# Kernel tuning notes

Measured on AMD Instinct MI355X. Metric: run time of the kernel, lower is better.

## Reference

```python
import jax, jax.numpy as jnp
import numpy as np


def mish(x):
    return x * jnp.tanh(jax.nn.softplus(x))


def setup_inputs() -> dict:
    key = jax.random.key(0)
    k1, k2, k3, k4, k5 = jax.random.split(key, 5)
    B, C, H, W = 16, 256, 128, 128
    sq = max(int(C * 4 * 0.25), 1)  # 256
    return {
        "t": jax.random.normal(k1, (B, C, H, W), dtype=jnp.float32),
        "w_reduce": jax.random.normal(k2, (sq, 4 * C), dtype=jnp.float32) * 0.02,
        "b_reduce": jax.random.normal(k3, (sq,), dtype=jnp.float32) * 0.02,
        "w_expand": jax.random.normal(k4, (4 * C, sq), dtype=jnp.float32) * 0.02,
        "b_expand": jax.random.normal(k5, (4 * C,), dtype=jnp.float32) * 0.02,
    }


def reference(t, w_reduce, b_reduce, w_expand, b_expand):
    B, C, H, W = t.shape
    h, w = H // 2, W // 2
    # Quadrants (views of t)
    x00 = t[:, :, :h, :w]
    x01 = t[:, :, :h, w:]
    x10 = t[:, :, h:, :w]
    x11 = t[:, :, h:, w:]
    # Squeeze: per-quadrant global average pool -> [B, 4C]
    means = jnp.concatenate(
        [q.mean(axis=(2, 3)) for q in (x00, x01, x10, x11)], axis=1
    )
    # 1x1 convs at 1x1 spatial == small GEMMs
    z = mish(means @ w_reduce.T + b_reduce)          # [B, sq]
    gate = jax.nn.sigmoid(z @ w_expand.T + b_expand)  # [B, 4C]
    g = gate.reshape(B, 4, C)[:, :, :, None, None]    # [B,4,C,1,1]
    # out2 = t * gate broadcast back into each quadrant (out=ones in source)
    top = jnp.concatenate([x00 * g[:, 0], x01 * g[:, 1]], axis=3)
    bot = jnp.concatenate([x10 * g[:, 2], x11 * g[:, 3]], axis=3)
    return jnp.concatenate([top, bot], axis=2)
```

## Files before the change

### kernel.cpp

```cpp
#include <hip/hip_runtime.h>
#include <math.h>

namespace {
constexpr int Bx = 16;
constexpr int Cx = 256;
constexpr int Hx = 128;
constexpr int Wx = 128;
constexpr int PLANE = Hx * Wx;
constexpr int NPLANES = Bx * Cx;
constexpr int SQ = 256;
constexpr int C4 = 4 * Cx;
}

__global__ __launch_bounds__(256) void k_qmeans(const float* __restrict__ t,
                                                float* __restrict__ means) {
    const int plane = blockIdx.x;
    const int tid = threadIdx.x;
    const float4* tp = (const float4*)(t + (size_t)plane * PLANE);

    float sTop = 0.f, sBot = 0.f;
#pragma unroll
    for (int i = 0; i < 8; ++i) {
        float4 d = tp[tid + 256 * i];
        sTop += (d.x + d.y) + (d.z + d.w);
    }
#pragma unroll
    for (int i = 8; i < 16; ++i) {
        float4 d = tp[tid + 256 * i];
        sBot += (d.x + d.y) + (d.z + d.w);
    }

#pragma unroll
    for (int m = 1; m <= 8; m <<= 1) {
        sTop += __shfl_xor(sTop, m);
        sBot += __shfl_xor(sBot, m);
    }
    sTop += __shfl_xor(sTop, 32);
    sBot += __shfl_xor(sBot, 32);

    __shared__ float red[4][4];
    const int lane = tid & 63;
    const int wave = tid >> 6;
    const int qc = (tid >> 4) & 1;
    if (lane == 0 || lane == 16) {
        red[qc][wave] = sTop;
        red[2 + qc][wave] = sBot;
    }
    __syncthreads();
    if (tid < 4) {
        const float s = red[tid][0] + red[tid][1] + red[tid][2] + red[tid][3];
        const int b = plane >> 8;
        const int c = plane & 255;
        means[b * C4 + tid * Cx + c] = s * (1.f / (64.f * 64.f));
    }
}

__global__ __launch_bounds__(256) void k_mlp(const float* __restrict__ means,
                                             const float* __restrict__ w_reduce,
                                             const float* __restrict__ b_reduce,
                                             const float* __restrict__ w_expand,
                                             const float* __restrict__ b_expand,
                                             float* __restrict__ gate) {
    const int b = blockIdx.x;
    const int tid = threadIdx.x;
    __shared__ __align__(16) float ms[C4];
    __shared__ __align__(16) float zs[SQ];

#pragma unroll
    for (int i = 0; i < 4; ++i)
        ms[tid + 256 * i] = means[b * C4 + tid + 256 * i];
    __syncthreads();

    {
        float acc = b_reduce[tid];
        const float4* wr = (const float4*)(w_reduce + (size_t)tid * C4);
        const float4* m4 = (const float4*)ms;
#pragma unroll 8
        for (int k = 0; k < C4 / 4; ++k) {
            const float4 w = wr[k];
            const float4 m = m4[k];
            acc += m.x * w.x + m.y * w.y + m.z * w.z + m.w * w.w;
        }
        const float sp = (acc > 20.f) ? acc : log1pf(expf(acc));
        zs[tid] = acc * tanhf(sp);
    }
    __syncthreads();

#pragma unroll
    for (int i = 0; i < 4; ++i) {
        const int j = tid + 256 * i;
        float acc = b_expand[j];
        const float4* we = (const float4*)(w_expand + (size_t)j * SQ);
        const float4* z4 = (const float4*)zs;
#pragma unroll 8
        for (int k = 0; k < SQ / 4; ++k) {
            const float4 w = we[k];
            const float4 z = z4[k];
            acc += z.x * w.x + z.y * w.y + z.z * w.z + z.w * w.w;
        }
        gate[b * C4 + j] = 1.f / (1.f + expf(-acc));
    }
}

__global__ __launch_bounds__(256) void k_apply(const float* __restrict__ t,
                                               const float* __restrict__ gate,
                                               float* __restrict__ out) {
    const int plane = blockIdx.x;
    const int tid = threadIdx.x;
    const int b = plane >> 8;
    const int c = plane & 255;

    const float g0 = gate[b * C4 + 0 * Cx + c];
    const float g1 = gate[b * C4 + 1 * Cx + c];
    const float g2 = gate[b * C4 + 2 * Cx + c];
    const float g3 = gate[b * C4 + 3 * Cx + c];
    const int qc = (tid >> 4) & 1;
    const float gTop = qc ? g1 : g0;
    const float gBot = qc ? g3 : g2;

    const float4* tp = (const float4*)(t + (size_t)plane * PLANE);
    float4* op = (float4*)((float*)out + (size_t)plane * PLANE);
#pragma unroll
    for (int i = 0; i < 16; ++i) {
        float4 d = tp[tid + 256 * i];
        const float g = (i < 8) ? gTop : gBot;
        d.x *= g; d.y *= g; d.z *= g; d.w *= g;
        op[tid + 256 * i] = d;
    }
}

extern "C" void kernel_launch(void* const* d_in, const int* in_sizes, int n_in,
                              void* d_out, int out_size, void* d_ws, size_t ws_size,
                              hipStream_t stream) {
    const float* t        = (const float*)d_in[0];
    const float* w_reduce = (const float*)d_in[1];
    const float* b_reduce = (const float*)d_in[2];
    const float* w_expand = (const float*)d_in[3];
    const float* b_expand = (const float*)d_in[4];
    float* out = (float*)d_out;

    float* means = (float*)d_ws;
    float* gate  = means + Bx * C4;

    k_qmeans<<<NPLANES, 256, 0, stream>>>(t, means);
    k_mlp<<<Bx, 256, 0, stream>>>(means, w_reduce, b_reduce, w_expand, b_expand, gate);
    k_apply<<<NPLANES, 256, 0, stream>>>(t, gate, out);
}
```

Measured before the change: 555.3 us.

## Fuse pool, MLP, and gating into one cooperative persistent kernel with reversed apply order

Replaces the three kernel launches with one cooperative kernel of 1024 blocks that does the quadrant pooling, then both MLP layers, then the gating multiply, with grid-wide syncs between phases. The expand GEMM is now split across 64 blocks instead of 16. The apply phase walks planes in reverse order so the most recently pooled planes, likely still in the last-level cache, are re-read first. The aims are to cut launch gaps and reuse cached input, at the cost of three grid barriers and only 64 of 1024 blocks doing the MLP work.

```diff
diff --git a/kernel.cpp b/kernel.cpp
--- a/kernel.cpp
+++ b/kernel.cpp
@@ -1,5 +1,8 @@
 #include <hip/hip_runtime.h>
+#include <hip/hip_cooperative_groups.h>
 #include <math.h>
+
+namespace cg = cooperative_groups;
 
 namespace {
 constexpr int Bx = 16;
@@ -10,71 +13,79 @@
 constexpr int NPLANES = Bx * Cx;
 constexpr int SQ = 256;
 constexpr int C4 = 4 * Cx;
+constexpr int NBLK = 1024;
+constexpr int PPB = NPLANES / NBLK;
 }
 
-__global__ __launch_bounds__(256) void k_qmeans(const float* __restrict__ t,
-                                                float* __restrict__ means) {
-    const int plane = blockIdx.x;
+__global__ __launch_bounds__(256, 4) void fused(
+    const float* __restrict__ t,
+    const float* __restrict__ w_reduce,
+    const float* __restrict__ b_reduce,
+    const float* __restrict__ w_expand,
+    const float* __restrict__ b_expand,
+    float* __restrict__ out,
+    float* __restrict__ ws) {
+    float* means = ws;
+    float* zbuf  = ws + Bx * C4;
+    float* gate  = zbuf + Bx * SQ;
+
+    cg::grid_group grid = cg::this_grid();
     const int tid = threadIdx.x;
-    const float4* tp = (const float4*)(t + (size_t)plane * PLANE);
 
-    float sTop = 0.f, sBot = 0.f;
+    __shared__ __align__(16) float sh[C4];
+    __shared__ float red[4][4];
+
+    for (int p = 0; p < PPB; ++p) {
+        const int plane = blockIdx.x * PPB + p;
+        const float4* tp = (const float4*)(t + (size_t)plane * PLANE);
+
+        float sTop = 0.f, sBot = 0.f;
 #pragma unroll
-    for (int i = 0; i < 8; ++i) {
-        float4 d = tp[tid + 256 * i];
-        sTop += (d.x + d.y) + (d.z + d.w);
+        for (int i = 0; i < 8; ++i) {
+            float4 d = tp[tid + 256 * i];
+            sTop += (d.x + d.y) + (d.z + d.w);
+        }
+#pragma unroll
+        for (int i = 8; i < 16; ++i) {
+            float4 d = tp[tid + 256 * i];
+            sBot += (d.x + d.y) + (d.z + d.w);
+        }
+#pragma unroll
+        for (int m = 1; m <= 8; m <<= 1) {
+            sTop += __shfl_xor(sTop, m);
+            sBot += __shfl_xor(sBot, m);
+        }
+        sTop += __shfl_xor(sTop, 32);
+        sBot += __shfl_xor(sBot, 32);
+
+        const int lane = tid & 63;
+        const int wave = tid >> 6;
+        const int qc = (tid >> 4) & 1;
+        if (lane == 0 || lane == 16) {
+            red[qc][wave] = sTop;
+            red[2 + qc][wave] = sBot;
+        }
+        __syncthreads();
+        if (tid < 4) {
+            const float s = red[tid][0] + red[tid][1] + red[tid][2] + red[tid][3];
+            const int b = plane >> 8;
+            const int c = plane & 255;
+            means[b * C4 + tid * Cx + c] = s * (1.f / (64.f * 64.f));
+        }
+        __syncthreads();
     }
+    grid.sync();
+
+    if (blockIdx.x < Bx) {
+        const int b = blockIdx.x;
 #pragma unroll
-    for (int i = 8; i < 16; ++i) {
-        float4 d = tp[tid + 256 * i];
-        sBot += (d.x + d.y) + (d.z + d.w);
-    }
+        for (int i = 0; i < 4; ++i)
+            sh[tid + 256 * i] = means[b * C4 + tid + 256 * i];
+        __syncthreads();
 
-#pragma unroll
-    for (int m = 1; m <= 8; m <<= 1) {
-        sTop += __shfl_xor(sTop, m);
-        sBot += __shfl_xor(sBot, m);
-    }
-    sTop += __shfl_xor(sTop, 32);
-    sBot += __shfl_xor(sBot, 32);
-
-    __shared__ float red[4][4];
-    const int lane = tid & 63;
-    const int wave = tid >> 6;
-    const int qc = (tid >> 4) & 1;
-    if (lane == 0 || lane == 16) {
-        red[qc][wave] = sTop;
-        red[2 + qc][wave] = sBot;
-    }
-    __syncthreads();
-    if (tid < 4) {
-        const float s = red[tid][0] + red[tid][1] + red[tid][2] + red[tid][3];
-        const int b = plane >> 8;
-        const int c = plane & 255;
-        means[b * C4 + tid * Cx + c] = s * (1.f / (64.f * 64.f));
-    }
-}
-
-__global__ __launch_bounds__(256) void k_mlp(const float* __restrict__ means,
-                                             const float* __restrict__ w_reduce,
-                                             const float* __restrict__ b_reduce,
-                                             const float* __restrict__ w_expand,
-                                             const float* __restrict__ b_expand,
-                                             float* __restrict__ gate) {
-    const int b = blockIdx.x;
-    const int tid = threadIdx.x;
-    __shared__ __align__(16) float ms[C4];
-    __shared__ __align__(16) float zs[SQ];
-
-#pragma unroll
-    for (int i = 0; i < 4; ++i)
-        ms[tid + 256 * i] = means[b * C4 + tid + 256 * i];
-    __syncthreads();
-
-    {
         float acc = b_reduce[tid];
         const float4* wr = (const float4*)(w_reduce + (size_t)tid * C4);
-        const float4* m4 = (const float4*)ms;
+        const float4* m4 = (const float4*)sh;
 #pragma unroll 8
         for (int k = 0; k < C4 / 4; ++k) {
             const float4 w = wr[k];
@@ -82,16 +93,19 @@
             acc += m.x * w.x + m.y * w.y + m.z * w.z + m.w * w.w;
         }
         const float sp = (acc > 20.f) ? acc : log1pf(expf(acc));
-        zs[tid] = acc * tanhf(sp);
+        zbuf[b * SQ + tid] = acc * tanhf(sp);
     }
-    __syncthreads();
+    grid.sync();
 
-#pragma unroll
-    for (int i = 0; i < 4; ++i) {
-        const int j = tid + 256 * i;
+    if (blockIdx.x < 4 * Bx) {
+        const int b = blockIdx.x >> 2;
+        const int j = ((blockIdx.x & 3) << 8) + tid;
+        sh[tid] = zbuf[b * SQ + tid];
+        __syncthreads();
+
         float acc = b_expand[j];
         const float4* we = (const float4*)(w_expand + (size_t)j * SQ);
-        const float4* z4 = (const float4*)zs;
+        const float4* z4 = (const float4*)sh;
 #pragma unroll 8
         for (int k = 0; k < SQ / 4; ++k) {
             const float4 w = we[k];
@@ -100,32 +114,30 @@
         }
         gate[b * C4 + j] = 1.f / (1.f + expf(-acc));
     }
-}
+    grid.sync();
 
-__global__ __launch_bounds__(256) void k_apply(const float* __restrict__ t,
-                                               const float* __restrict__ gate,
-                                               float* __restrict__ out) {
-    const int plane = blockIdx.x;
-    const int tid = threadIdx.x;
-    const int b = plane >> 8;
-    const int c = plane & 255;
+    for (int p = 0; p < PPB; ++p) {
+        const int plane = (NPLANES - 1) - (blockIdx.x * PPB + p);
+        const int b = plane >> 8;
+        const int c = plane & 255;
 
-    const float g0 = gate[b * C4 + 0 * Cx + c];
-    const float g1 = gate[b * C4 + 1 * Cx + c];
-    const float g2 = gate[b * C4 + 2 * Cx + c];
-    const float g3 = gate[b * C4 + 3 * Cx + c];
-    const int qc = (tid >> 4) & 1;
-    const float gTop = qc ? g1 : g0;
-    const float gBot = qc ? g3 : g2;
+        const float g0 = gate[b * C4 + 0 * Cx + c];
+        const float g1 = gate[b * C4 + 1 * Cx + c];
+        const float g2 = gate[b * C4 + 2 * Cx + c];
+        const float g3 = gate[b * C4 + 3 * Cx + c];
+        const int qc = (tid >> 4) & 1;
+        const float gTop = qc ? g1 : g0;
+        const float gBot = qc ? g3 : g2;
 
-    const float4* tp = (const float4*)(t + (size_t)plane * PLANE);
-    float4* op = (float4*)((float*)out + (size_t)plane * PLANE);
+        const float4* tp = (const float4*)(t + (size_t)plane * PLANE);
+        float4* op = (float4*)(out + (size_t)plane * PLANE);
 #pragma unroll
-    for (int i = 0; i < 16; ++i) {
-        float4 d = tp[tid + 256 * i];
-        const float g = (i < 8) ? gTop : gBot;
-        d.x *= g; d.y *= g; d.z *= g; d.w *= g;
-        op[tid + 256 * i] = d;
+        for (int i = 0; i < 16; ++i) {
+            float4 d = tp[tid + 256 * i];
+            const float g = (i < 8) ? gTop : gBot;
+            d.x *= g; d.y *= g; d.z *= g; d.w *= g;
+            op[tid + 256 * i] = d;
+        }
     }
 }
 
@@ -138,11 +150,10 @@
     const float* w_expand = (const float*)d_in[3];
     const float* b_expand = (const float*)d_in[4];
     float* out = (float*)d_out;
+    float* ws  = (float*)d_ws;
 
-    float* means = (float*)d_ws;
-    float* gate  = means + Bx * C4;
-
-    k_qmeans<<<NPLANES, 256, 0, stream>>>(t, means);
-    k_mlp<<<Bx, 256, 0, stream>>>(means, w_reduce, b_reduce, w_expand, b_expand, gate);
-    k_apply<<<NPLANES, 256, 0, stream>>>(t, gate, out);
+    void* args[] = {(void*)&t, (void*)&w_reduce, (void*)&b_reduce,
+                    (void*)&w_expand, (void*)&b_expand, (void*)&out, (void*)&ws};
+    hipLaunchCooperativeKernel((const void*)fused, dim3(NBLK), dim3(256),
+                               args, 0, stream);
 }
```

Result: slower. 891.3 us (+60.5%).
